# Optimization experiments

Measured on AMD Instinct MI355X. Metric: run time of the kernel, lower is better.

The kernel has to match this reference:

```python
import jax, jax.numpy as jnp
import numpy as np

N, C, H, W = 4, 64, 64, 64
K = 3


def _unfold(x, k):
    """torch F.unfold with padding k//2: [n,c,h,w] -> [n, c*k*k, h*w].
    Feature ordering matches torch: index = c*k*k + i*k + j."""
    p = k // 2
    n, c, h, w = x.shape
    xp = jnp.pad(x, ((0, 0), (0, 0), (p, p), (p, p)))
    patches = jnp.stack(
        [xp[:, :, i:i + h, j:j + w] for i in range(k) for j in range(k)], axis=2
    )  # [n, c, k*k, h, w]
    return patches.reshape(n, c * k * k, h * w)


def _mask_vec(c, k):
    # causal patch mask from __init__: zero out center-and-right of middle row and all rows below
    m = np.ones((c, k, k), np.float32)
    m[:, k // 2, k // 2:] = 0
    m[:, k // 2 + 1:, :] = 0
    return jnp.asarray(m.reshape(1, c * k * k, 1))


def setup_inputs() -> dict:
    key = jax.random.key(0)
    k1, k2 = jax.random.split(key)
    y_hat = jax.random.normal(k1, (N, C, H, W), dtype=jnp.float32)
    y_prob = jax.random.uniform(k2, (N, 1, H, W), dtype=jnp.float32)
    return {"y_hat": y_hat, "y_prob": y_prob}


def reference(y_hat, y_prob):
    k = K
    n, c, h, w = y_hat.shape
    L = h * w
    mask = _mask_vec(c, k)

    u = _unfold(y_hat, k) * mask                              # [n, c*k*k, L]
    u = u / jnp.maximum(jnp.linalg.norm(u, axis=1, keepdims=True), 1e-12)
    R = jnp.einsum('nfl,nfm->nlm', u, u)                      # [n, L, L] cosine sims

    # eval path: keep strictly-upper triangle (causal: l < m)
    row = jnp.arange(L)[:, None]
    col = jnp.arange(L)[None, :]
    R = jnp.where(col > row, R, 0.0)

    R_star = jnp.max(R, axis=1)                               # [n, L]
    arg = jnp.argmax(R, axis=1).astype(jnp.int32)             # [n, L]

    y_unf = _unfold(y_hat, k)                                 # [n, c*k*k, L]
    ref_unfold = jnp.take_along_axis(y_unf, arg[:, None, :], axis=2)

    prob_unf = y_prob.reshape(n, -1, L)                       # 1x1 unfold
    U_unf = jnp.take_along_axis(prob_unf, arg[:, None, :], axis=2)

    S = R_star.reshape(n, 1, h, w)
    U = U_unf.reshape(n, -1, h, w)

    # eval-mode position-0 overrides
    S = S.at[:, :, 0, 0].set(1e-8)
    U = U.at[:, :, 0, 0].set(1e-8)
    ref_unfold = ref_unfold.at[:, :, 0].set(0.0)
    arg = arg.at[:, 0].set(-1)

    S = jnp.clip(S, 1e-8, 1.0)
    U = jnp.clip(U, 1e-8, 1.0)
    return S, U, ref_unfold, arg
```

## Files before the change

### kernel.cpp

```cpp
#include <hip/hip_runtime.h>
#include <stdint.h>

#define Nn 4
#define Cc 64
#define LL 4096
#define KK 256
#define TRI2 528

typedef _Float16 half8 __attribute__((ext_vector_type(8)));
typedef float f32x16 __attribute__((ext_vector_type(16)));
typedef float f32x4 __attribute__((ext_vector_type(4)));
typedef unsigned short ushort8v __attribute__((ext_vector_type(8)));

__device__ __forceinline__ unsigned f2ord(float f) {
    unsigned u = __float_as_uint(f);
    return u ^ ((u & 0x80000000u) ? 0xFFFFFFFFu : 0x80000000u);
}
__device__ __forceinline__ float ord2f(unsigned o) {
    unsigned u = (o & 0x80000000u) ? (o ^ 0x80000000u) : ~o;
    return __uint_as_float(u);
}
__device__ __forceinline__ unsigned short h2u(_Float16 h) {
    union { _Float16 f; unsigned short u; } x; x.f = h; return x.u;
}

__global__ __launch_bounds__(256) void build_v(const float* __restrict__ yhat,
                                               unsigned short* __restrict__ VhT,
                                               unsigned short* __restrict__ VlT,
                                               float* __restrict__ yhatT,
                                               unsigned long long* __restrict__ best) {
    int blk = blockIdx.x;
    int xcd = blk & 7;
    int n = xcd >> 1;
    int i64 = (blk >> 3) + (xcd & 1) * 128;
    int tid = threadIdx.x;
    if (tid < 16) best[(size_t)n * LL + i64 * 16 + tid] = 0ull;

    int cg = tid & 15;
    int l = i64 * 16 + (tid >> 4);
    int y = l >> 6, x = l & 63;
    const float* src = yhat + (size_t)n * (Cc * LL);

    float vals[16];
    float ctr[4];
    float sumsq = 0.f;
#pragma unroll
    for (int ci = 0; ci < 4; ++ci) {
        const float* p = src + (cg * 4 + ci) * LL;
        float t0 = (y > 0 && x > 0)  ? p[l - 65] : 0.f;
        float t1 = (y > 0)           ? p[l - 64] : 0.f;
        float t2 = (y > 0 && x < 63) ? p[l - 63] : 0.f;
        float t3 = (x > 0)           ? p[l - 1]  : 0.f;
        ctr[ci] = p[l];
        vals[ci * 4 + 0] = t0; vals[ci * 4 + 1] = t1;
        vals[ci * 4 + 2] = t2; vals[ci * 4 + 3] = t3;
        sumsq += t0 * t0 + t1 * t1 + t2 * t2 + t3 * t3;
    }
    sumsq += __shfl_xor(sumsq, 1, 64);
    sumsq += __shfl_xor(sumsq, 2, 64);
    sumsq += __shfl_xor(sumsq, 4, 64);
    sumsq += __shfl_xor(sumsq, 8, 64);
    float inv = 1.f / fmaxf(sqrtf(sumsq), 1e-12f);

    f32x4 cv; cv.x = ctr[0]; cv.y = ctr[1]; cv.z = ctr[2]; cv.w = ctr[3];
    *(f32x4*)(yhatT + ((size_t)n * LL + l) * 64 + cg * 4) = cv;

    size_t pk = ((((size_t)n * 128 + (l >> 5)) * 16 + cg) << 9) + (l & 31) * 8;
    unsigned short* dh = VhT + pk;
    unsigned short* dl = VlT + pk;
    ushort8v hA, hB, lA, lB;
#pragma unroll
    for (int kk = 0; kk < 16; ++kk) {
        float v = vals[kk] * inv;
        _Float16 h = (fabsf(v) < 6.1035e-5f) ? (_Float16)0 : (_Float16)v;
        _Float16 lo = (_Float16)((v - (float)h) * 2048.0f);
        unsigned short hu = h2u(h * (_Float16)2048.0f);
        unsigned short lu = h2u(lo);
        if (kk < 8) { hA[kk] = hu; lA[kk] = lu; }
        else        { hB[kk - 8] = hu; lB[kk - 8] = lu; }
    }
    *(ushort8v*)(dh)       = hA;
    *(ushort8v*)(dh + 256) = hB;
    *(ushort8v*)(dl)       = lA;
    *(ushort8v*)(dl + 256) = lB;
}

__device__ __forceinline__ void mfmaset(half8 (&al)[2][2], half8 (&ah)[2][2],
                                        half8 (&bl)[2][2], half8 (&bh)[2][2],
                                        f32x16 (&acc)[2][2]) {
    __builtin_amdgcn_s_setprio(1);
#pragma unroll
    for (int kc = 0; kc < 2; ++kc)
#pragma unroll
        for (int r = 0; r < 2; ++r)
#pragma unroll
            for (int c = 0; c < 2; ++c)
                acc[r][c] = __builtin_amdgcn_mfma_f32_32x32x16_f16(al[r][kc], bh[c][kc], acc[r][c], 0, 0, 0);
#pragma unroll
    for (int kc = 0; kc < 2; ++kc)
#pragma unroll
        for (int r = 0; r < 2; ++r)
#pragma unroll
            for (int c = 0; c < 2; ++c)
                acc[r][c] = __builtin_amdgcn_mfma_f32_32x32x16_f16(ah[r][kc], bl[c][kc], acc[r][c], 0, 0, 0);
#pragma unroll
    for (int kc = 0; kc < 2; ++kc)
#pragma unroll
        for (int r = 0; r < 2; ++r)
#pragma unroll
            for (int c = 0; c < 2; ++c)
                acc[r][c] = __builtin_amdgcn_mfma_f32_32x32x16_f16(ah[r][kc], bh[c][kc], acc[r][c], 0, 0, 0);
    __builtin_amdgcn_s_setprio(0);
}

__global__ __launch_bounds__(256) void simmax(const unsigned short* __restrict__ Vh,
                                              const unsigned short* __restrict__ Vl,
                                              unsigned long long* __restrict__ best) {
    __shared__ __align__(16) unsigned short S[32768];

    int bx = blockIdx.x;
    int xcd = bx & 7, idx = bx >> 3;
    int n = xcd >> 1;
    int t = (xcd & 1) * 264 + idx;
    int j = (int)((sqrtf(8.f * (float)t + 1.f) - 1.f) * 0.5f);
    while ((j + 1) * (j + 2) / 2 <= t) ++j;
    while (j * (j + 1) / 2 > t) --j;
    int i = t - j * (j + 1) / 2;
    int l0 = i * 128, m0 = j * 128;

    int tid = threadIdx.x;
    int w = tid >> 6, lane = tid & 63;
    int r5 = lane & 31, h5 = lane >> 5;
    int rw = (w & 1) * 64;
    int cw = (w >> 1) * 64;
    bool skip = (i == j) && (rw == 64) && (cw == 0);

    const unsigned short* VhB = Vh + (size_t)n * (LL * KK);
    const unsigned short* VlB = Vl + (size_t)n * (LL * KK);

    int aRow0 = l0 >> 5;
    int bRow0 = m0 >> 5;

    const unsigned short* gsrc[8];
    int lslot[8];
#pragma unroll
    for (int q = 0; q < 8; ++q) {
        int c = w * 8 + q;
        int side = c >> 4, rb = (c >> 2) & 3, lo = (c >> 1) & 1, kc = c & 1;
        int rowblk = (side ? bRow0 : aRow0) + rb;
        const unsigned short* base = lo ? VlB : VhB;
        gsrc[q] = base + (((size_t)rowblk * 16 + kc) << 9) + lane * 8;
        lslot[q] = c * 512;
    }

    int arb = (w & 1) * 2;
    int brb = (w >> 1) * 2;

    f32x16 acc[2][2];
#pragma unroll
    for (int r = 0; r < 2; ++r)
#pragma unroll
        for (int c = 0; c < 2; ++c) acc[r][c] = (f32x16)0.f;

#pragma unroll
    for (int q = 0; q < 8; ++q)
        __builtin_amdgcn_global_load_lds(
            (const __attribute__((address_space(1))) void*)(gsrc[q]),
            (__attribute__((address_space(3))) void*)(S + lslot[q]), 16, 0, 0);
    __syncthreads();

#pragma unroll
    for (int kt = 0; kt < 8; ++kt) {
        const int cur = (kt & 1) * 16384;
        const int nxt = 16384 - cur;

        if (kt < 7) {
            const size_t kadv = (size_t)(kt + 1) * 1024;
#pragma unroll
            for (int q = 0; q < 8; ++q)
                __builtin_amdgcn_global_load_lds(
                    (const __attribute__((address_space(1))) void*)(gsrc[q] + kadv),
                    (__attribute__((address_space(3))) void*)(S + nxt + lslot[q]), 16, 0, 0);
        }

        if (!skip) {
            half8 al[2][2], ah[2][2], bl[2][2], bh[2][2];
#pragma unroll
            for (int kc = 0; kc < 2; ++kc)
#pragma unroll
                for (int r = 0; r < 2; ++r) {
                    al[r][kc] = *(const half8*)(S + cur + ((arb + r) * 4 + 2 + kc) * 512 + lane * 8);
                    bh[r][kc] = *(const half8*)(S + cur + (16 + (brb + r) * 4 + kc) * 512 + lane * 8);
                }
#pragma unroll
            for (int kc = 0; kc < 2; ++kc)
#pragma unroll
                for (int r = 0; r < 2; ++r) {
                    ah[r][kc] = *(const half8*)(S + cur + ((arb + r) * 4 + kc) * 512 + lane * 8);
                    bl[r][kc] = *(const half8*)(S + cur + (16 + (brb + r) * 4 + 2 + kc) * 512 + lane * 8);
                }
            mfmaset(al, ah, bl, bh, acc);
        }

        if (kt < 7) __syncthreads();
    }

    if (skip) return;
    unsigned long long* bb = best + (size_t)n * LL;
    const float s = 1.f / 4194304.f;
#pragma unroll
    for (int c = 0; c < 2; ++c) {
        int m = m0 + cw + c * 32 + r5;
        unsigned long long key = 0ull;
#pragma unroll
        for (int r = 0; r < 2; ++r)
#pragma unroll
            for (int g = 0; g < 16; ++g) {
                int l = l0 + rw + r * 32 + (g & 3) + 8 * (g >> 2) + 4 * h5;
                if (l < m) {
                    float v = acc[r][c][g] * s;
                    unsigned long long k2 =
                        ((unsigned long long)f2ord(v) << 32) |
                        (unsigned long long)(0xFFFFFFFFu - (unsigned)l);
                    key = (k2 > key) ? k2 : key;
                }
            }
        unsigned long long o = __shfl_xor(key, 32, 64);
        key = (o > key) ? o : key;
        if (h5 == 0 && key != 0ull) atomicMax(bb + m, key);
    }
}

__global__ __launch_bounds__(256) void writeout(const float* __restrict__ yhatT,
                                                const float* __restrict__ yprob,
                                                const unsigned long long* __restrict__ best,
                                                float* __restrict__ out) {
    __shared__ float P[576 * 17];

    int blk = blockIdx.x;
    int xcd = blk & 7;
    int n = xcd >> 1;
    int mb = (blk >> 3) + (xcd & 1) * 128;
    int m0 = mb * 16;
    int tid = threadIdx.x;
    int ml = tid >> 4;
    int cs = (tid & 15) * 4;
    int m = m0 + ml;

    unsigned long long key = best[(size_t)n * LL + m];
    unsigned l = 0xFFFFFFFFu - (unsigned)(key & 0xFFFFFFFFull);
    float val = ord2f((unsigned)(key >> 32));
    bool zero = (m == 0);
    if (zero) l = 0;
    int ly = (int)(l >> 6), lx = (int)(l & 63);

    float* Sout = out;
    float* Uout = out + 16384;
    float* Rout = out + 32768;
    float* Aout = out + 9469952;

    if (cs == 0) {
        float S = zero ? 1e-8f : fminf(fmaxf(val, 1e-8f), 1.0f);
        float U = zero ? 1e-8f : fminf(fmaxf(yprob[(size_t)n * LL + l], 1e-8f), 1.0f);
        Sout[(size_t)n * LL + m] = S;
        Uout[(size_t)n * LL + m] = U;
        Aout[(size_t)n * LL + m] = zero ? -1.0f : (float)l;
    }

    const float* T = yhatT + ((size_t)n * LL) * 64;
#pragma unroll
    for (int i = 0; i < 3; ++i) {
        int yy = ly + i - 1;
        bool rok = (!zero) && (yy >= 0) && (yy < 64);
#pragma unroll
        for (int jj = 0; jj < 3; ++jj) {
            int xx = lx + jj - 1;
            f32x4 v; v.x = 0.f; v.y = 0.f; v.z = 0.f; v.w = 0.f;
            if (rok && xx >= 0 && xx < 64)
                v = *(const f32x4*)(T + ((size_t)(yy * 64 + xx)) * 64 + cs);
            int ij = i * 3 + jj;
            P[((cs + 0) * 9 + ij) * 17 + ml] = v.x;
            P[((cs + 1) * 9 + ij) * 17 + ml] = v.y;
            P[((cs + 2) * 9 + ij) * 17 + ml] = v.z;
            P[((cs + 3) * 9 + ij) * 17 + ml] = v.w;
        }
    }
    __syncthreads();

    float* R = Rout + (size_t)n * (576 * LL) + m0;
    int fl = tid >> 4;
    int mm2 = tid & 15;
#pragma unroll 1
    for (int it2 = 0; it2 < 36; ++it2) {
        int f = it2 * 16 + fl;
        float v = P[f * 17 + mm2];
        __builtin_nontemporal_store(v, R + (size_t)f * LL + mm2);
    }
}

extern "C" void kernel_launch(void* const* d_in, const int* in_sizes, int n_in,
                              void* d_out, int out_size, void* d_ws, size_t ws_size,
                              hipStream_t stream) {
    const float* yhat  = (const float*)d_in[0];
    const float* yprob = (const float*)d_in[1];
    float* out = (float*)d_out;

    unsigned short* VhT = (unsigned short*)d_ws;
    unsigned short* VlT = (unsigned short*)((char*)d_ws + 8388608);
    unsigned long long* best =
        (unsigned long long*)((char*)d_ws + 16777216);
    float* yhatT = (float*)((char*)d_ws + 16908288);

    build_v<<<1024, 256, 0, stream>>>(yhat, VhT, VlT, yhatT, best);
    simmax<<<Nn * TRI2, 256, 0, stream>>>(VhT, VlT, best);
    writeout<<<1024, 256, 0, stream>>>(yhatT, yprob, best, out);
}
```

Measured before the change: 153.5 us.

## Use triple-buffered half-K-step LDS pipeline with partial vmcnt barriers in simmax

The simmax GEMM loop now loads each K step in two half-size chunks into a three-slot LDS ring (48KB instead of 64KB). Barriers wait with vmcnt(4), so one chunk's prefetch stays in flight while the current chunk is consumed. The MFMA sequence is split so the al*bh products of each half run as soon as that half arrives, and the remaining products run after the second half. This aims to overlap global-to-LDS loads with MFMA work and to reduce LDS use for higher occupancy, at the cost of twice as many barriers and hand-written waitcnt logic that depends on how the compiler orders the loads.

```diff
diff --git a/kernel.cpp b/kernel.cpp
--- a/kernel.cpp
+++ b/kernel.cpp
@@ -22,6 +22,17 @@
 }
 __device__ __forceinline__ unsigned short h2u(_Float16 h) {
     union { _Float16 f; unsigned short u; } x; x.f = h; return x.u;
+}
+
+__device__ __forceinline__ void pipe_barrier_vm4() {
+    asm volatile("s_waitcnt lgkmcnt(0) vmcnt(4)" ::: "memory");
+    __builtin_amdgcn_s_barrier();
+    __builtin_amdgcn_sched_barrier(0);
+}
+__device__ __forceinline__ void pipe_barrier_vm0() {
+    asm volatile("s_waitcnt lgkmcnt(0) vmcnt(0)" ::: "memory");
+    __builtin_amdgcn_s_barrier();
+    __builtin_amdgcn_sched_barrier(0);
 }
 
 __global__ __launch_bounds__(256) void build_v(const float* __restrict__ yhat,
@@ -85,38 +96,10 @@
     *(ushort8v*)(dl + 256) = lB;
 }
 
-__device__ __forceinline__ void mfmaset(half8 (&al)[2][2], half8 (&ah)[2][2],
-                                        half8 (&bl)[2][2], half8 (&bh)[2][2],
-                                        f32x16 (&acc)[2][2]) {
-    __builtin_amdgcn_s_setprio(1);
-#pragma unroll
-    for (int kc = 0; kc < 2; ++kc)
-#pragma unroll
-        for (int r = 0; r < 2; ++r)
-#pragma unroll
-            for (int c = 0; c < 2; ++c)
-                acc[r][c] = __builtin_amdgcn_mfma_f32_32x32x16_f16(al[r][kc], bh[c][kc], acc[r][c], 0, 0, 0);
-#pragma unroll
-    for (int kc = 0; kc < 2; ++kc)
-#pragma unroll
-        for (int r = 0; r < 2; ++r)
-#pragma unroll
-            for (int c = 0; c < 2; ++c)
-                acc[r][c] = __builtin_amdgcn_mfma_f32_32x32x16_f16(ah[r][kc], bl[c][kc], acc[r][c], 0, 0, 0);
-#pragma unroll
-    for (int kc = 0; kc < 2; ++kc)
-#pragma unroll
-        for (int r = 0; r < 2; ++r)
-#pragma unroll
-            for (int c = 0; c < 2; ++c)
-                acc[r][c] = __builtin_amdgcn_mfma_f32_32x32x16_f16(ah[r][kc], bh[c][kc], acc[r][c], 0, 0, 0);
-    __builtin_amdgcn_s_setprio(0);
-}
-
 __global__ __launch_bounds__(256) void simmax(const unsigned short* __restrict__ Vh,
                                               const unsigned short* __restrict__ Vl,
                                               unsigned long long* __restrict__ best) {
-    __shared__ __align__(16) unsigned short S[32768];
+    __shared__ __align__(16) unsigned short S[24576];
 
     int bx = blockIdx.x;
     int xcd = bx & 7, idx = bx >> 3;
@@ -141,16 +124,15 @@
     int aRow0 = l0 >> 5;
     int bRow0 = m0 >> 5;
 
-    const unsigned short* gsrc[8];
-    int lslot[8];
-#pragma unroll
-    for (int q = 0; q < 8; ++q) {
-        int c = w * 8 + q;
-        int side = c >> 4, rb = (c >> 2) & 3, lo = (c >> 1) & 1, kc = c & 1;
+    const unsigned short* gsrc[4];
+    int lslot[4];
+#pragma unroll
+    for (int q = 0; q < 4; ++q) {
+        int cidx = w * 4 + q;
+        int side = cidx >> 3, rb = (cidx >> 1) & 3, lo = cidx & 1;
         int rowblk = (side ? bRow0 : aRow0) + rb;
-        const unsigned short* base = lo ? VlB : VhB;
-        gsrc[q] = base + (((size_t)rowblk * 16 + kc) << 9) + lane * 8;
-        lslot[q] = c * 512;
+        gsrc[q] = (lo ? VlB : VhB) + ((size_t)(rowblk * 16) << 9) + lane * 8;
+        lslot[q] = cidx * 512;
     }
 
     int arb = (w & 1) * 2;
@@ -162,48 +144,86 @@
 #pragma unroll
         for (int c = 0; c < 2; ++c) acc[r][c] = (f32x16)0.f;
 
-#pragma unroll
-    for (int q = 0; q < 8; ++q)
-        __builtin_amdgcn_global_load_lds(
-            (const __attribute__((address_space(1))) void*)(gsrc[q]),
-            (__attribute__((address_space(3))) void*)(S + lslot[q]), 16, 0, 0);
-    __syncthreads();
+#define GLDS(KQ, BN)                                                              \
+    do {                                                                          \
+        _Pragma("unroll")                                                         \
+        for (int q = 0; q < 4; ++q)                                               \
+            __builtin_amdgcn_global_load_lds(                                     \
+                (const __attribute__((address_space(1))) void*)(gsrc[q] + (size_t)(KQ) * 512), \
+                (__attribute__((address_space(3))) void*)(S + (BN) * 8192 + lslot[q]), 16, 0, 0); \
+    } while (0)
+
+    GLDS(0, 0);
+    GLDS(1, 1);
 
 #pragma unroll
     for (int kt = 0; kt < 8; ++kt) {
-        const int cur = (kt & 1) * 16384;
-        const int nxt = 16384 - cur;
-
-        if (kt < 7) {
-            const size_t kadv = (size_t)(kt + 1) * 1024;
-#pragma unroll
-            for (int q = 0; q < 8; ++q)
-                __builtin_amdgcn_global_load_lds(
-                    (const __attribute__((address_space(1))) void*)(gsrc[q] + kadv),
-                    (__attribute__((address_space(3))) void*)(S + nxt + lslot[q]), 16, 0, 0);
+        const int b0 = (2 * kt) % 3;
+        const int b1 = (2 * kt + 1) % 3;
+
+        half8 al[2][2], ah[2][2], bl[2][2], bh[2][2];
+
+        pipe_barrier_vm4();
+        if (kt < 7) GLDS(2 * kt + 2, (2 * kt + 2) % 3);
+        if (!skip) {
+#pragma unroll
+            for (int r = 0; r < 2; ++r) {
+                al[r][0] = *(const half8*)(S + b0 * 8192 + ((arb + r) * 2 + 1) * 512 + lane * 8);
+                bh[r][0] = *(const half8*)(S + b0 * 8192 + (8 + (brb + r) * 2) * 512 + lane * 8);
+            }
+#pragma unroll
+            for (int r = 0; r < 2; ++r) {
+                ah[r][0] = *(const half8*)(S + b0 * 8192 + ((arb + r) * 2) * 512 + lane * 8);
+                bl[r][0] = *(const half8*)(S + b0 * 8192 + (9 + (brb + r) * 2) * 512 + lane * 8);
+            }
+            __builtin_amdgcn_s_setprio(1);
+#pragma unroll
+            for (int r = 0; r < 2; ++r)
+#pragma unroll
+                for (int c = 0; c < 2; ++c)
+                    acc[r][c] = __builtin_amdgcn_mfma_f32_32x32x16_f16(al[r][0], bh[c][0], acc[r][c], 0, 0, 0);
+            __builtin_amdgcn_s_setprio(0);
         }
 
+        if (kt < 7) pipe_barrier_vm4();
+        else        pipe_barrier_vm0();
+        if (kt < 7) GLDS(2 * kt + 3, (2 * kt + 3) % 3);
+
         if (!skip) {
-            half8 al[2][2], ah[2][2], bl[2][2], bh[2][2];
+#pragma unroll
+            for (int r = 0; r < 2; ++r) {
+                al[r][1] = *(const half8*)(S + b1 * 8192 + ((arb + r) * 2 + 1) * 512 + lane * 8);
+                bh[r][1] = *(const half8*)(S + b1 * 8192 + (8 + (brb + r) * 2) * 512 + lane * 8);
+            }
+#pragma unroll
+            for (int r = 0; r < 2; ++r) {
+                ah[r][1] = *(const half8*)(S + b1 * 8192 + ((arb + r) * 2) * 512 + lane * 8);
+                bl[r][1] = *(const half8*)(S + b1 * 8192 + (9 + (brb + r) * 2) * 512 + lane * 8);
+            }
+            __builtin_amdgcn_s_setprio(1);
+#pragma unroll
+            for (int r = 0; r < 2; ++r)
+#pragma unroll
+                for (int c = 0; c < 2; ++c)
+                    acc[r][c] = __builtin_amdgcn_mfma_f32_32x32x16_f16(al[r][1], bh[c][1], acc[r][c], 0, 0, 0);
 #pragma unroll
             for (int kc = 0; kc < 2; ++kc)
 #pragma unroll
-                for (int r = 0; r < 2; ++r) {
-                    al[r][kc] = *(const half8*)(S + cur + ((arb + r) * 4 + 2 + kc) * 512 + lane * 8);
-                    bh[r][kc] = *(const half8*)(S + cur + (16 + (brb + r) * 4 + kc) * 512 + lane * 8);
-                }
+                for (int r = 0; r < 2; ++r)
+#pragma unroll
+                    for (int c = 0; c < 2; ++c)
+                        acc[r][c] = __builtin_amdgcn_mfma_f32_32x32x16_f16(ah[r][kc], bl[c][kc], acc[r][c], 0, 0, 0);
 #pragma unroll
             for (int kc = 0; kc < 2; ++kc)
 #pragma unroll
-                for (int r = 0; r < 2; ++r) {
-                    ah[r][kc] = *(const half8*)(S + cur + ((arb + r) * 4 + kc) * 512 + lane * 8);
-                    bl[r][kc] = *(const half8*)(S + cur + (16 + (brb + r) * 4 + 2 + kc) * 512 + lane * 8);
-                }
-            mfmaset(al, ah, bl, bh, acc);
+                for (int r = 0; r < 2; ++r)
+#pragma unroll
+                    for (int c = 0; c < 2; ++c)
+                        acc[r][c] = __builtin_amdgcn_mfma_f32_32x32x16_f16(ah[r][kc], bh[c][kc], acc[r][c], 0, 0, 0);
+            __builtin_amdgcn_s_setprio(0);
         }
-
-        if (kt < 7) __syncthreads();
-    }
+    }
+#undef GLDS
 
     if (skip) return;
     unsigned long long* bb = best + (size_t)n * LL;
```

After: 152.7 us. No clear change (-0.5%).
